# Optimization experiments

Hardware: AMD Instinct MI355X
Metric: run time of the kernel (lower is better)

The kernel has to match this reference:

```python
import jax, jax.numpy as jnp
import numpy as np

N_NODES = 20000
N_EDGES = 320000
IN_F = 256
OUT_F = 64
HEADS = 4
ALPHA = 0.1  # leaky_relu negative slope


def setup_inputs() -> dict:
    key = jax.random.key(0)
    ks = jax.random.split(key, 8)
    return {
        "input1": jax.random.normal(ks[0], (N_NODES, IN_F), jnp.float32),
        "input2": jax.random.normal(ks[1], (N_NODES, IN_F), jnp.float32),
        # per-head params: Ws maps source feats -> target_out, Wt maps target feats -> source_out
        "Ws": jax.random.normal(ks[2], (HEADS, IN_F, OUT_F), jnp.float32) * 0.06,
        "Wt": jax.random.normal(ks[3], (HEADS, IN_F, OUT_F), jnp.float32) * 0.06,
        "a1": jax.random.normal(ks[4], (HEADS, 2 * OUT_F), jnp.float32) * 0.1,
        "a2": jax.random.normal(ks[5], (HEADS, 2 * OUT_F), jnp.float32) * 0.1,
        # COO nonzeros of A_opt [n_target, n_source]
        "tgt_idx": jax.random.randint(ks[6], (N_EDGES,), 0, N_NODES),
        "src_idx": jax.random.randint(ks[7], (N_EDGES,), 0, N_NODES),
    }


def _segment_softmax(scores, seg, num_segments):
    m = jax.lax.stop_gradient(jax.ops.segment_max(scores, seg, num_segments=num_segments))
    w = jnp.exp(scores - m[seg])
    d = jax.ops.segment_sum(w, seg, num_segments=num_segments)
    d = jnp.where(d == 0, 1.0, d)
    return w / d[seg]


def _head(x1, x2, Ws, Wt, a1, a2, src, tgt, n_s, n_t):
    s = x1 @ Ws  # [n_s, OUT_F]  messages source -> target
    t = x2 @ Wt  # [n_t, OUT_F]  messages target -> source
    out = Ws.shape[1]
    # edge score e = leaky_relu(a^T [s_src || t_tgt]); split a to avoid edge-level concat
    e1 = jax.nn.leaky_relu((s @ a1[:out])[src] + (t @ a1[out:])[tgt], ALPHA)
    e2 = jax.nn.leaky_relu((s @ a2[:out])[src] + (t @ a2[out:])[tgt], ALPHA)
    alpha_ts = _segment_softmax(e1, tgt, n_t)  # softmax over sources per target
    alpha_st = _segment_softmax(e2, src, n_s)  # softmax over targets per source
    h_ts = jax.ops.segment_sum(alpha_ts[:, None] * s[src], tgt, num_segments=n_t)
    h_st = jax.ops.segment_sum(alpha_st[:, None] * t[tgt], src, num_segments=n_s)
    return jax.nn.elu(h_st), jax.nn.elu(h_ts)  # concat=True -> ELU per head


def reference(input1, input2, Ws, Wt, a1, a2, tgt_idx, src_idx):
    n_s, n_t = input1.shape[0], input2.shape[0]
    head_fn = jax.vmap(
        lambda W1, W2, v1, v2: _head(input1, input2, W1, W2, v1, v2, src_idx, tgt_idx, n_s, n_t)
    )
    h_st, h_ts = head_fn(Ws, Wt, a1, a2)  # each [H, n, OUT_F]
    h_st = jnp.transpose(h_st, (1, 0, 2)).reshape(n_s, -1)  # concat heads
    h_ts = jnp.transpose(h_ts, (1, 0, 2)).reshape(n_t, -1)
    return h_st, h_ts
```

## Files before the change

kernel.cpp:

```cpp
#include <hip/hip_runtime.h>
#include <math.h>

#define N_NODES 20000
#define N_EDGES 320000
#define IN_F 256
#define OUT_F 64
#define HEADS 4
#define NCOL 256
#define LRELU_ALPHA 0.1f
#define ELL_CAP 64

#define SCAT_BLOCKS 640
#define SCAT_THREADS (SCAT_BLOCKS * 256)

#define WRES_BLOCKS 128
#define LDS_STRIDE 264

#define AGG_BLOCKS 2048

typedef __attribute__((ext_vector_type(8))) short short8;
typedef __attribute__((ext_vector_type(4))) float floatx4;

__device__ __forceinline__ float lrelu(float x) {
    return x > 0.f ? x : LRELU_ALPHA * x;
}
__device__ __forceinline__ unsigned short f2bf(float f) {
    unsigned int u = __float_as_uint(f);
    u = (u + 0x7FFF + ((u >> 16) & 1)) >> 16;
    return (unsigned short)u;
}
__device__ __forceinline__ float bf2f(unsigned short u) {
    return __uint_as_float(((unsigned int)u) << 16);
}

__global__ __launch_bounds__(256) void prep_w_kernel(
    const float* __restrict__ Ws, const float* __restrict__ Wt,
    unsigned short* __restrict__ Wsb, unsigned short* __restrict__ Wtb,
    int* __restrict__ cnt)
{
    const int gid = blockIdx.x * 256 + threadIdx.x;

    for (int i = gid; i < 2 * N_NODES; i += 16384) cnt[i] = 0;

    const int mat = gid >> 13;
    const int r   = gid & 8191;
    const int kc  = r >> 8;
    const int c   = r & 255;
    const float* W    = mat ? Wt : Ws;
    unsigned short* O = mat ? Wtb : Wsb;
    const int h = c >> 6, j = c & 63;
    const int k0 = kc * 8;
    unsigned short v[8] __attribute__((aligned(16)));
#pragma unroll
    for (int i = 0; i < 8; ++i)
        v[i] = f2bf(W[(size_t)h * (IN_F * OUT_F) + (size_t)(k0 + i) * OUT_F + j]);
    *(uint4*)(O + (size_t)c * IN_F + k0) = *(const uint4*)v;
}

__global__ __launch_bounds__(256) void scatter_kernel(
    const int* __restrict__ src, const int* __restrict__ tgt,
    int* __restrict__ cnt_t, int* __restrict__ cnt_s,
    unsigned short* __restrict__ elist_t, unsigned short* __restrict__ elist_s)
{
    const int e0 = blockIdx.x * 256 + threadIdx.x;
    const int e1 = e0 + SCAT_THREADS;
    const bool h1 = e1 < N_EDGES;

    int s0 = src[e0], t0 = tgt[e0];
    int s1 = 0, t1 = 0;
    if (h1) { s1 = src[e1]; t1 = tgt[e1]; }

    int p0 = atomicAdd(&cnt_t[t0], 1);
    int q0 = atomicAdd(&cnt_s[s0], 1);
    int p1 = 0, q1 = 0;
    if (h1) {
        p1 = atomicAdd(&cnt_t[t1], 1);
        q1 = atomicAdd(&cnt_s[s1], 1);
    }

    if (p0 < ELL_CAP) elist_t[t0 * ELL_CAP + p0] = (unsigned short)s0;
    if (q0 < ELL_CAP) elist_s[s0 * ELL_CAP + q0] = (unsigned short)t0;
    if (h1) {
        if (p1 < ELL_CAP) elist_t[t1 * ELL_CAP + p1] = (unsigned short)s1;
        if (q1 < ELL_CAP) elist_s[s1 * ELL_CAP + q1] = (unsigned short)t1;
    }
}

__global__ __launch_bounds__(1024, 4) void gemm_wres_kernel(
    const float* __restrict__ A0, const unsigned short* __restrict__ Wb0,
    const float* __restrict__ A1, const unsigned short* __restrict__ Wb1,
    unsigned short* __restrict__ C0, unsigned short* __restrict__ C1,
    const float* __restrict__ a1, const float* __restrict__ a2,
    float* __restrict__ ss1, float* __restrict__ ss2,
    float* __restrict__ tt1, float* __restrict__ tt2)
{
    const int tid = threadIdx.x;
    const float* A           = (blockIdx.y == 0) ? A0 : A1;
    const unsigned short* Wb = (blockIdx.y == 0) ? Wb0 : Wb1;
    unsigned short* C        = (blockIdx.y == 0) ? C0 : C1;

    __shared__ __align__(16) unsigned short Bl[256][LDS_STRIDE];

    for (int i = tid; i < 8192; i += 1024) {
        const int n  = i >> 5;
        const int kc = (i & 31) << 3;
        *(uint4*)&Bl[n][kc] = *(const uint4*)(Wb + (size_t)n * IN_F + kc);
    }
    __syncthreads();

    const int lane = tid & 63;
    const int w    = tid >> 6;
    const int quad = lane >> 4;
    const int l15  = lane & 15;
    const int g    = blockIdx.x * 16 + w;

    if (g >= 1250) return;

    const float* arow = A + (size_t)(g * 16 + l15) * IN_F + quad * 8;

    float4 ua[8];
#pragma unroll
    for (int kk = 0; kk < 4; ++kk) {
        ua[2 * kk]     = *(const float4*)(arow + kk * 32);
        ua[2 * kk + 1] = *(const float4*)(arow + kk * 32 + 4);
    }
    short8 af[4];
#pragma unroll
    for (int kk = 0; kk < 4; ++kk) {
        short8 t;
        t[0] = (short)f2bf(ua[2 * kk].x);     t[1] = (short)f2bf(ua[2 * kk].y);
        t[2] = (short)f2bf(ua[2 * kk].z);     t[3] = (short)f2bf(ua[2 * kk].w);
        t[4] = (short)f2bf(ua[2 * kk + 1].x); t[5] = (short)f2bf(ua[2 * kk + 1].y);
        t[6] = (short)f2bf(ua[2 * kk + 1].z); t[7] = (short)f2bf(ua[2 * kk + 1].w);
        af[kk] = t;
    }

    float4 ub[8];
#pragma unroll
    for (int kk = 0; kk < 4; ++kk) {
        ub[2 * kk]     = *(const float4*)(arow + (kk + 4) * 32);
        ub[2 * kk + 1] = *(const float4*)(arow + (kk + 4) * 32 + 4);
    }

    floatx4 acc[16];
#pragma unroll
    for (int c = 0; c < 16; ++c) acc[c] = (floatx4){0.f, 0.f, 0.f, 0.f};

#pragma unroll
    for (int kk = 0; kk < 4; ++kk) {
#pragma unroll
        for (int c = 0; c < 16; ++c) {
            short8 bfrag = *(const short8*)&Bl[c * 16 + l15][kk * 32 + quad * 8];
            acc[c] = __builtin_amdgcn_mfma_f32_16x16x32_bf16(af[kk], bfrag, acc[c], 0, 0, 0);
        }
    }

#pragma unroll
    for (int kk = 0; kk < 4; ++kk) {
        short8 t;
        t[0] = (short)f2bf(ub[2 * kk].x);     t[1] = (short)f2bf(ub[2 * kk].y);
        t[2] = (short)f2bf(ub[2 * kk].z);     t[3] = (short)f2bf(ub[2 * kk].w);
        t[4] = (short)f2bf(ub[2 * kk + 1].x); t[5] = (short)f2bf(ub[2 * kk + 1].y);
        t[6] = (short)f2bf(ub[2 * kk + 1].z); t[7] = (short)f2bf(ub[2 * kk + 1].w);
        af[kk] = t;
    }
#pragma unroll
    for (int kk = 0; kk < 4; ++kk) {
#pragma unroll
        for (int c = 0; c < 16; ++c) {
            short8 bfrag = *(const short8*)&Bl[c * 16 + l15][(kk + 4) * 32 + quad * 8];
            acc[c] = __builtin_amdgcn_mfma_f32_16x16x32_bf16(af[kk], bfrag, acc[c], 0, 0, 0);
        }
    }

#pragma unroll
    for (int c = 0; c < 16; ++c) {
        const int col = c * 16 + l15;
#pragma unroll
        for (int r = 0; r < 4; ++r) {
            const int m = g * 16 + quad * 4 + r;
            C[(size_t)m * NCOL + col] = f2bf(acc[c][r]);
        }
    }

    const int off_aj = (blockIdx.y == 0) ? 0 : 64;
    float* o1 = (blockIdx.y == 0) ? ss1 : tt1;
    float* o2 = (blockIdx.y == 0) ? ss2 : tt2;

    float p1[4][4] = {{0.f,0.f,0.f,0.f},{0.f,0.f,0.f,0.f},{0.f,0.f,0.f,0.f},{0.f,0.f,0.f,0.f}};
    float p2[4][4] = {{0.f,0.f,0.f,0.f},{0.f,0.f,0.f,0.f},{0.f,0.f,0.f,0.f},{0.f,0.f,0.f,0.f}};
#pragma unroll
    for (int c = 0; c < 16; ++c) {
        const int hh = c >> 2;
        const int jj = (c & 3) * 16 + l15;
        const float w1 = a1[hh * 128 + off_aj + jj];
        const float w2 = a2[hh * 128 + off_aj + jj];
#pragma unroll
        for (int r = 0; r < 4; ++r) {
            p1[hh][r] += acc[c][r] * w1;
            p2[hh][r] += acc[c][r] * w2;
        }
    }
#pragma unroll
    for (int m = 1; m < 16; m <<= 1) {
#pragma unroll
        for (int hh = 0; hh < 4; ++hh)
#pragma unroll
            for (int r = 0; r < 4; ++r) {
                p1[hh][r] += __shfl_xor(p1[hh][r], m, 64);
                p2[hh][r] += __shfl_xor(p2[hh][r], m, 64);
            }
    }
    if (l15 == 0) {
#pragma unroll
        for (int r = 0; r < 4; ++r) {
            const int m = g * 16 + quad * 4 + r;
#pragma unroll
            for (int hh = 0; hh < 4; ++hh) {
                o1[m * HEADS + hh] = p1[hh][r];
                o2[m * HEADS + hh] = p2[hh][r];
            }
        }
    }
}

__global__ __launch_bounds__(256) void agg_kernel(
    const int* __restrict__ cnt_t, const unsigned short* __restrict__ elist_t,
    const int* __restrict__ cnt_s, const unsigned short* __restrict__ elist_s,
    const float* __restrict__ ss1, const float* __restrict__ ss2,
    const float* __restrict__ tt1, const float* __restrict__ tt2,
    const unsigned short* __restrict__ s_bf, const unsigned short* __restrict__ t_bf,
    float* __restrict__ h_st, float* __restrict__ h_ts)
{
    const int b     = blockIdx.x;
    const int slice = b & 7;
    const int dir   = slice >> 2;
    const int h     = slice & 3;
    const int idx   = b >> 3;
    const int wave  = threadIdx.x >> 6;
    const int lane  = threadIdx.x & 63;
    const int quad  = lane >> 4;
    const int l15   = lane & 15;
    const int coff  = h * 64 + l15 * 4;

    const int*            cnt   = dir ? cnt_s   : cnt_t;
    const unsigned short* list  = dir ? elist_s : elist_t;
    const unsigned short* table = dir ? t_bf    : s_bf;
    const float*          nsc   = dir ? ss2     : tt1;
    const float*          esc   = dir ? tt2     : ss1;
    float*                outp  = dir ? h_st    : h_ts;

    const int nstart = (idx * N_NODES) >> 8;
    const int nend   = ((idx + 1) * N_NODES) >> 8;

    for (int n = nstart + wave; n < nend; n += 4) {
        const float base = nsc[n * HEADS + h];
        int deg = cnt[n];
        if (deg > ELL_CAP) deg = ELL_CAP;
        const unsigned short* lp = list + n * ELL_CAP;

        float4 acc = make_float4(0.f, 0.f, 0.f, 0.f);
        float den = 0.f;

        int p = quad;
        for (; p + 4 < deg; p += 8) {
            int m0 = lp[p], m1 = lp[p + 4];
            float e0 = esc[m0 * HEADS + h];
            float e1 = esc[m1 * HEADS + h];
            ushort4 r0 = *(const ushort4*)(table + (size_t)m0 * NCOL + coff);
            ushort4 r1 = *(const ushort4*)(table + (size_t)m1 * NCOL + coff);
            float w0 = __expf(lrelu(e0 + base));
            float w1 = __expf(lrelu(e1 + base));
            den += w0 + w1;
            acc.x += w0 * bf2f(r0.x) + w1 * bf2f(r1.x);
            acc.y += w0 * bf2f(r0.y) + w1 * bf2f(r1.y);
            acc.z += w0 * bf2f(r0.z) + w1 * bf2f(r1.z);
            acc.w += w0 * bf2f(r0.w) + w1 * bf2f(r1.w);
        }
        if (p < deg) {
            int m0 = lp[p];
            float w0 = __expf(lrelu(esc[m0 * HEADS + h] + base));
            ushort4 r0 = *(const ushort4*)(table + (size_t)m0 * NCOL + coff);
            den += w0;
            acc.x += w0 * bf2f(r0.x);
            acc.y += w0 * bf2f(r0.y);
            acc.z += w0 * bf2f(r0.z);
            acc.w += w0 * bf2f(r0.w);
        }

#pragma unroll
        for (int msk = 16; msk < 64; msk <<= 1) {
            den   += __shfl_xor(den,   msk, 64);
            acc.x += __shfl_xor(acc.x, msk, 64);
            acc.y += __shfl_xor(acc.y, msk, 64);
            acc.z += __shfl_xor(acc.z, msk, 64);
            acc.w += __shfl_xor(acc.w, msk, 64);
        }

        if (quad == 0) {
            if (den == 0.f) den = 1.f;
            float inv = 1.f / den;
            float4 r;
            r.x = acc.x * inv; r.y = acc.y * inv;
            r.z = acc.z * inv; r.w = acc.w * inv;
            r.x = (r.x > 0.f) ? r.x : expm1f(r.x);
            r.y = (r.y > 0.f) ? r.y : expm1f(r.y);
            r.z = (r.z > 0.f) ? r.z : expm1f(r.z);
            r.w = (r.w > 0.f) ? r.w : expm1f(r.w);
            *(float4*)(outp + (size_t)n * NCOL + coff) = r;
        }
    }
}

extern "C" void kernel_launch(void* const* d_in, const int* in_sizes, int n_in,
                              void* d_out, int out_size, void* d_ws, size_t ws_size,
                              hipStream_t stream)
{
    const float* input1 = (const float*)d_in[0];
    const float* input2 = (const float*)d_in[1];
    const float* Ws     = (const float*)d_in[2];
    const float* Wt     = (const float*)d_in[3];
    const float* a1     = (const float*)d_in[4];
    const float* a2     = (const float*)d_in[5];
    const int*   tgt    = (const int*)d_in[6];
    const int*   src    = (const int*)d_in[7];

    float* out  = (float*)d_out;
    float* h_st = out;
    float* h_ts = out + (size_t)N_NODES * NCOL;

    unsigned short* s_bf = (unsigned short*)d_ws;
    unsigned short* t_bf = s_bf + (size_t)N_NODES * NCOL;
    unsigned short* Wsb  = t_bf + (size_t)N_NODES * NCOL;
    unsigned short* Wtb  = Wsb + 256 * 256;
    float* ss1  = (float*)(Wtb + 256 * 256);
    float* ss2  = ss1 + N_NODES * HEADS;
    float* tt1  = ss2 + N_NODES * HEADS;
    float* tt2  = tt1 + N_NODES * HEADS;
    int*   cnt_t = (int*)(tt2 + N_NODES * HEADS);
    int*   cnt_s = cnt_t + N_NODES;
    unsigned short* elist_t = (unsigned short*)(cnt_s + N_NODES);
    unsigned short* elist_s = elist_t + (size_t)N_NODES * ELL_CAP;

    prep_w_kernel<<<64, 256, 0, stream>>>(Ws, Wt, Wsb, Wtb, cnt_t);

    scatter_kernel<<<SCAT_BLOCKS, 256, 0, stream>>>(src, tgt, cnt_t, cnt_s,
                                                    elist_t, elist_s);

    dim3 ggrid(WRES_BLOCKS, 2);
    gemm_wres_kernel<<<ggrid, 1024, 0, stream>>>(input1, Wsb, input2, Wtb,
                                                 s_bf, t_bf, a1, a2,
                                                 ss1, ss2, tt1, tt2);

    agg_kernel<<<AGG_BLOCKS, 256, 0, stream>>>(cnt_t, elist_t, cnt_s, elist_s,
                                               ss1, ss2, tt1, tt2, s_bf, t_bf, h_st, h_ts);
}
```

Baseline: 219.2 us.

## Split GEMM output columns across blocks, use 16-lane groups per node in aggregation

The GEMM now launches 512-thread blocks that each compute half of the 256 output columns (two heads), halving the LDS weight tile and the accumulator register count. This raises occupancy and the number of blocks, but the A rows are read twice. The aggregation kernel assigns each node to a 16-lane group that walks its whole edge list with 4-way unrolling, removing the cross-quad shuffle reduction in exchange for longer serial per-node loops. The scatter kernel is simplified to one edge per thread.

```diff
diff --git a/kernel.cpp b/kernel.cpp
--- a/kernel.cpp
+++ b/kernel.cpp
@@ -10,12 +10,9 @@
 #define LRELU_ALPHA 0.1f
 #define ELL_CAP 64
 
-#define SCAT_BLOCKS 640
-#define SCAT_THREADS (SCAT_BLOCKS * 256)
-
-#define WRES_BLOCKS 128
-#define LDS_STRIDE 264
-
+#define SCAT_BLOCKS 1250
+
+#define GEMM_GB 157
 #define AGG_BLOCKS 2048
 
 typedef __attribute__((ext_vector_type(8))) short short8;
@@ -62,31 +59,15 @@
     int* __restrict__ cnt_t, int* __restrict__ cnt_s,
     unsigned short* __restrict__ elist_t, unsigned short* __restrict__ elist_s)
 {
-    const int e0 = blockIdx.x * 256 + threadIdx.x;
-    const int e1 = e0 + SCAT_THREADS;
-    const bool h1 = e1 < N_EDGES;
-
-    int s0 = src[e0], t0 = tgt[e0];
-    int s1 = 0, t1 = 0;
-    if (h1) { s1 = src[e1]; t1 = tgt[e1]; }
-
-    int p0 = atomicAdd(&cnt_t[t0], 1);
-    int q0 = atomicAdd(&cnt_s[s0], 1);
-    int p1 = 0, q1 = 0;
-    if (h1) {
-        p1 = atomicAdd(&cnt_t[t1], 1);
-        q1 = atomicAdd(&cnt_s[s1], 1);
-    }
-
-    if (p0 < ELL_CAP) elist_t[t0 * ELL_CAP + p0] = (unsigned short)s0;
-    if (q0 < ELL_CAP) elist_s[s0 * ELL_CAP + q0] = (unsigned short)t0;
-    if (h1) {
-        if (p1 < ELL_CAP) elist_t[t1 * ELL_CAP + p1] = (unsigned short)s1;
-        if (q1 < ELL_CAP) elist_s[s1 * ELL_CAP + q1] = (unsigned short)t1;
-    }
-}
-
-__global__ __launch_bounds__(1024, 4) void gemm_wres_kernel(
+    const int e = blockIdx.x * 256 + threadIdx.x;
+    const int s = src[e], t = tgt[e];
+    const int p = atomicAdd(&cnt_t[t], 1);
+    const int q = atomicAdd(&cnt_s[s], 1);
+    if (p < ELL_CAP) elist_t[t * ELL_CAP + p] = (unsigned short)s;
+    if (q < ELL_CAP) elist_s[s * ELL_CAP + q] = (unsigned short)t;
+}
+
+__global__ __launch_bounds__(512, 4) void gemm_wres_kernel(
     const float* __restrict__ A0, const unsigned short* __restrict__ Wb0,
     const float* __restrict__ A1, const unsigned short* __restrict__ Wb1,
     unsigned short* __restrict__ C0, unsigned short* __restrict__ C1,
@@ -94,17 +75,19 @@
     float* __restrict__ ss1, float* __restrict__ ss2,
     float* __restrict__ tt1, float* __restrict__ tt2)
 {
-    const int tid = threadIdx.x;
+    const int tid  = threadIdx.x;
+    const int half = blockIdx.x & 1;
+    const int gb   = blockIdx.x >> 1;
     const float* A           = (blockIdx.y == 0) ? A0 : A1;
     const unsigned short* Wb = (blockIdx.y == 0) ? Wb0 : Wb1;
     unsigned short* C        = (blockIdx.y == 0) ? C0 : C1;
 
-    __shared__ __align__(16) unsigned short Bl[256][LDS_STRIDE];
-
-    for (int i = tid; i < 8192; i += 1024) {
+    __shared__ __align__(16) unsigned short Bl[128][264];
+
+    for (int i = tid; i < 4096; i += 512) {
         const int n  = i >> 5;
         const int kc = (i & 31) << 3;
-        *(uint4*)&Bl[n][kc] = *(const uint4*)(Wb + (size_t)n * IN_F + kc);
+        *(uint4*)&Bl[n][kc] = *(const uint4*)(Wb + (size_t)(half * 128 + n) * IN_F + kc);
     }
     __syncthreads();
 
@@ -112,8 +95,7 @@
     const int w    = tid >> 6;
     const int quad = lane >> 4;
     const int l15  = lane & 15;
-    const int g    = blockIdx.x * 16 + w;
-
+    const int g    = gb * 8 + w;
     if (g >= 1250) return;
 
     const float* arow = A + (size_t)(g * 16 + l15) * IN_F + quad * 8;
@@ -142,14 +124,14 @@
         ub[2 * kk + 1] = *(const float4*)(arow + (kk + 4) * 32 + 4);
     }
 
-    floatx4 acc[16];
-#pragma unroll
-    for (int c = 0; c < 16; ++c) acc[c] = (floatx4){0.f, 0.f, 0.f, 0.f};
-
-#pragma unroll
-    for (int kk = 0; kk < 4; ++kk) {
-#pragma unroll
-        for (int c = 0; c < 16; ++c) {
+    floatx4 acc[8];
+#pragma unroll
+    for (int c = 0; c < 8; ++c) acc[c] = (floatx4){0.f, 0.f, 0.f, 0.f};
+
+#pragma unroll
+    for (int kk = 0; kk < 4; ++kk) {
+#pragma unroll
+        for (int c = 0; c < 8; ++c) {
             short8 bfrag = *(const short8*)&Bl[c * 16 + l15][kk * 32 + quad * 8];
             acc[c] = __builtin_amdgcn_mfma_f32_16x16x32_bf16(af[kk], bfrag, acc[c], 0, 0, 0);
         }
@@ -167,15 +149,15 @@
 #pragma unroll
     for (int kk = 0; kk < 4; ++kk) {
 #pragma unroll
-        for (int c = 0; c < 16; ++c) {
+        for (int c = 0; c < 8; ++c) {
             short8 bfrag = *(const short8*)&Bl[c * 16 + l15][(kk + 4) * 32 + quad * 8];
             acc[c] = __builtin_amdgcn_mfma_f32_16x16x32_bf16(af[kk], bfrag, acc[c], 0, 0, 0);
         }
     }
 
 #pragma unroll
-    for (int c = 0; c < 16; ++c) {
-        const int col = c * 16 + l15;
+    for (int c = 0; c < 8; ++c) {
+        const int col = half * 128 + c * 16 + l15;
 #pragma unroll
         for (int r = 0; r < 4; ++r) {
             const int m = g * 16 + quad * 4 + r;
@@ -187,28 +169,29 @@
     float* o1 = (blockIdx.y == 0) ? ss1 : tt1;
     float* o2 = (blockIdx.y == 0) ? ss2 : tt2;
 
-    float p1[4][4] = {{0.f,0.f,0.f,0.f},{0.f,0.f,0.f,0.f},{0.f,0.f,0.f,0.f},{0.f,0.f,0.f,0.f}};
-    float p2[4][4] = {{0.f,0.f,0.f,0.f},{0.f,0.f,0.f,0.f},{0.f,0.f,0.f,0.f},{0.f,0.f,0.f,0.f}};
-#pragma unroll
-    for (int c = 0; c < 16; ++c) {
-        const int hh = c >> 2;
+    float p1[2][4] = {{0.f,0.f,0.f,0.f},{0.f,0.f,0.f,0.f}};
+    float p2[2][4] = {{0.f,0.f,0.f,0.f},{0.f,0.f,0.f,0.f}};
+#pragma unroll
+    for (int c = 0; c < 8; ++c) {
+        const int hl = c >> 2;
+        const int hh = half * 2 + hl;
         const int jj = (c & 3) * 16 + l15;
         const float w1 = a1[hh * 128 + off_aj + jj];
         const float w2 = a2[hh * 128 + off_aj + jj];
 #pragma unroll
         for (int r = 0; r < 4; ++r) {
-            p1[hh][r] += acc[c][r] * w1;
-            p2[hh][r] += acc[c][r] * w2;
+            p1[hl][r] += acc[c][r] * w1;
+            p2[hl][r] += acc[c][r] * w2;
         }
     }
 #pragma unroll
     for (int m = 1; m < 16; m <<= 1) {
 #pragma unroll
-        for (int hh = 0; hh < 4; ++hh)
+        for (int hl = 0; hl < 2; ++hl)
 #pragma unroll
             for (int r = 0; r < 4; ++r) {
-                p1[hh][r] += __shfl_xor(p1[hh][r], m, 64);
-                p2[hh][r] += __shfl_xor(p2[hh][r], m, 64);
+                p1[hl][r] += __shfl_xor(p1[hl][r], m, 64);
+                p2[hl][r] += __shfl_xor(p2[hl][r], m, 64);
             }
     }
     if (l15 == 0) {
@@ -216,9 +199,10 @@
         for (int r = 0; r < 4; ++r) {
             const int m = g * 16 + quad * 4 + r;
 #pragma unroll
-            for (int hh = 0; hh < 4; ++hh) {
-                o1[m * HEADS + hh] = p1[hh][r];
-                o2[m * HEADS + hh] = p2[hh][r];
+            for (int hl = 0; hl < 2; ++hl) {
+                const int hh = half * 2 + hl;
+                o1[m * HEADS + hh] = p1[hl][r];
+                o2[m * HEADS + hh] = p2[hl][r];
             }
         }
     }
@@ -237,10 +221,8 @@
     const int dir   = slice >> 2;
     const int h     = slice & 3;
     const int idx   = b >> 3;
-    const int wave  = threadIdx.x >> 6;
-    const int lane  = threadIdx.x & 63;
-    const int quad  = lane >> 4;
-    const int l15   = lane & 15;
+    const int qg    = threadIdx.x >> 4;
+    const int l15   = threadIdx.x & 15;
     const int coff  = h * 64 + l15 * 4;
 
     const int*            cnt   = dir ? cnt_s   : cnt_t;
@@ -250,10 +232,12 @@
     const float*          esc   = dir ? tt2     : ss1;
     float*                outp  = dir ? h_st    : h_ts;
 
+    const float* esch = esc + h;
+
     const int nstart = (idx * N_NODES) >> 8;
     const int nend   = ((idx + 1) * N_NODES) >> 8;
 
-    for (int n = nstart + wave; n < nend; n += 4) {
+    for (int n = nstart + qg; n < nend; n += 16) {
         const float base = nsc[n * HEADS + h];
         int deg = cnt[n];
         if (deg > ELL_CAP) deg = ELL_CAP;
@@ -262,24 +246,29 @@
         float4 acc = make_float4(0.f, 0.f, 0.f, 0.f);
         float den = 0.f;
 
-        int p = quad;
-        for (; p + 4 < deg; p += 8) {
-            int m0 = lp[p], m1 = lp[p + 4];
-            float e0 = esc[m0 * HEADS + h];
-            float e1 = esc[m1 * HEADS + h];
+        int p = 0;
+        for (; p + 3 < deg; p += 4) {
+            int m0 = lp[p],     m1 = lp[p + 1];
+            int m2 = lp[p + 2], m3 = lp[p + 3];
+            float e0 = esch[m0 * HEADS], e1 = esch[m1 * HEADS];
+            float e2 = esch[m2 * HEADS], e3 = esch[m3 * HEADS];
             ushort4 r0 = *(const ushort4*)(table + (size_t)m0 * NCOL + coff);
             ushort4 r1 = *(const ushort4*)(table + (size_t)m1 * NCOL + coff);
+            ushort4 r2 = *(const ushort4*)(table + (size_t)m2 * NCOL + coff);
+            ushort4 r3 = *(const ushort4*)(table + (size_t)m3 * NCOL + coff);
             float w0 = __expf(lrelu(e0 + base));
             float w1 = __expf(lrelu(e1 + base));
-            den += w0 + w1;
-            acc.x += w0 * bf2f(r0.x) + w1 * bf2f(r1.x);
-            acc.y += w0 * bf2f(r0.y) + w1 * bf2f(r1.y);
-            acc.z += w0 * bf2f(r0.z) + w1 * bf2f(r1.z);
-            acc.w += w0 * bf2f(r0.w) + w1 * bf2f(r1.w);
-        }
-        if (p < deg) {
+            float w2 = __expf(lrelu(e2 + base));
+            float w3 = __expf(lrelu(e3 + base));
+            den += (w0 + w1) + (w2 + w3);
+            acc.x += (w0 * bf2f(r0.x) + w1 * bf2f(r1.x)) + (w2 * bf2f(r2.x) + w3 * bf2f(r3.x));
+            acc.y += (w0 * bf2f(r0.y) + w1 * bf2f(r1.y)) + (w2 * bf2f(r2.y) + w3 * bf2f(r3.y));
+            acc.z += (w0 * bf2f(r0.z) + w1 * bf2f(r1.z)) + (w2 * bf2f(r2.z) + w3 * bf2f(r3.z));
+            acc.w += (w0 * bf2f(r0.w) + w1 * bf2f(r1.w)) + (w2 * bf2f(r2.w) + w3 * bf2f(r3.w));
+        }
+        for (; p < deg; ++p) {
             int m0 = lp[p];
-            float w0 = __expf(lrelu(esc[m0 * HEADS + h] + base));
+            float w0 = __expf(lrelu(esch[m0 * HEADS] + base));
             ushort4 r0 = *(const ushort4*)(table + (size_t)m0 * NCOL + coff);
             den += w0;
             acc.x += w0 * bf2f(r0.x);
@@ -288,27 +277,16 @@
             acc.w += w0 * bf2f(r0.w);
         }
 
-#pragma unroll
-        for (int msk = 16; msk < 64; msk <<= 1) {
-            den   += __shfl_xor(den,   msk, 64);
-            acc.x += __shfl_xor(acc.x, msk, 64);
-            acc.y += __shfl_xor(acc.y, msk, 64);
-            acc.z += __shfl_xor(acc.z, msk, 64);
-            acc.w += __shfl_xor(acc.w, msk, 64);
-        }
-
-        if (quad == 0) {
-            if (den == 0.f) den = 1.f;
-            float inv = 1.f / den;
-            float4 r;
-            r.x = acc.x * inv; r.y = acc.y * inv;
-            r.z = acc.z * inv; r.w = acc.w * inv;
-            r.x = (r.x > 0.f) ? r.x : expm1f(r.x);
-            r.y = (r.y > 0.f) ? r.y : expm1f(r.y);
-            r.z = (r.z > 0.f) ? r.z : expm1f(r.z);
-            r.w = (r.w > 0.f) ? r.w : expm1f(r.w);
-            *(float4*)(outp + (size_t)n * NCOL + coff) = r;
-        }
+        if (den == 0.f) den = 1.f;
+        float inv = 1.f / den;
+        float4 r;
+        r.x = acc.x * inv; r.y = acc.y * inv;
+        r.z = acc.z * inv; r.w = acc.w * inv;
+        r.x = (r.x > 0.f) ? r.x : expm1f(r.x);
+        r.y = (r.y > 0.f) ? r.y : expm1f(r.y);
+        r.z = (r.z > 0.f) ? r.z : expm1f(r.z);
+        r.w = (r.w > 0.f) ? r.w : expm1f(r.w);
+        *(float4*)(outp + (size_t)n * NCOL + coff) = r;
     }
 }
 
@@ -347,10 +325,10 @@
     scatter_kernel<<<SCAT_BLOCKS, 256, 0, stream>>>(src, tgt, cnt_t, cnt_s,
                                                     elist_t, elist_s);
 
-    dim3 ggrid(WRES_BLOCKS, 2);
-    gemm_wres_kernel<<<ggrid, 1024, 0, stream>>>(input1, Wsb, input2, Wtb,
-                                                 s_bf, t_bf, a1, a2,
-                                                 ss1, ss2, tt1, tt2);
+    dim3 ggrid(GEMM_GB * 2, 2);
+    gemm_wres_kernel<<<ggrid, 512, 0, stream>>>(input1, Wsb, input2, Wtb,
+                                                s_bf, t_bf, a1, a2,
+                                                ss1, ss2, tt1, tt2);
 
     agg_kernel<<<AGG_BLOCKS, 256, 0, stream>>>(cnt_t, elist_t, cnt_s, elist_s,
                                                ss1, ss2, tt1, tt2, s_bf, t_bf, h_st, h_ts);
```

New measurement: 205.5 us. -6.2%, faster.
